# Kernel optimization log

Hardware: AMD Instinct MI355X
Metric: run time of the kernel (lower is better)

Reference implementation:

```python
import jax, jax.numpy as jnp
import numpy as np

N_NODES = 50000
N_EDGES = 800000
N_GRAPHS = 500
DIM = 64
RBF_DIM = 5      # ceil(cutoff/width) = ceil(5.0/1)
N_CONV = 3
N_TYPES = 100
CLS_DIM = 2000
CUTOFF = 5.0

def _w(key, shape, fan_in):
    return jax.random.normal(key, shape, dtype=jnp.float32) / np.sqrt(fan_in)

def setup_inputs() -> dict:
    key = jax.random.key(0)
    ks = jax.random.split(key, 16)
    return {
        "node_types": jax.random.randint(ks[0], (N_NODES,), 0, N_TYPES, dtype=jnp.int32),
        "edge_src": jax.random.randint(ks[1], (N_EDGES,), 0, N_NODES, dtype=jnp.int32),
        "edge_dst": jax.random.randint(ks[2], (N_EDGES,), 0, N_NODES, dtype=jnp.int32),
        "graph_ids": jnp.sort(jax.random.randint(ks[3], (N_NODES,), 0, N_GRAPHS, dtype=jnp.int32)),
        "distance": jax.random.uniform(ks[4], (N_EDGES,), dtype=jnp.float32) * CUTOFF,
        "emb": jax.random.normal(ks[5], (N_TYPES, DIM), dtype=jnp.float32),
        "conv_w1": _w(ks[6], (N_CONV, DIM, DIM), DIM),
        "cf1_w": _w(ks[7], (N_CONV, RBF_DIM, DIM), RBF_DIM),
        "cf1_b": jnp.zeros((N_CONV, DIM), jnp.float32),
        "cf2_w": _w(ks[8], (N_CONV, DIM, DIM), DIM),
        "cf2_b": jnp.zeros((N_CONV, DIM), jnp.float32),
        "nl2_w": _w(ks[9], (N_CONV, DIM, DIM), DIM),
        "nl2_b": jnp.zeros((N_CONV, DIM), jnp.float32),
        "nl3_w": _w(ks[10], (N_CONV, DIM, DIM), DIM),
        "nl3_b": jnp.zeros((N_CONV, DIM), jnp.float32),
        "d1_w": _w(ks[11], (DIM, 256), DIM),
        "d1_b": jnp.zeros((256,), jnp.float32),
        "d2_w": _w(ks[12], (256, 256), 256),
        "d2_b": jnp.zeros((256,), jnp.float32),
        "cls_w": _w(ks[13], (256, CLS_DIM), 256),
        "cls_b": jnp.zeros((CLS_DIM,), jnp.float32),
        "ac_w": _w(ks[14], (256, N_TYPES), 256),
        "ac_b": jnp.zeros((N_TYPES,), jnp.float32),
    }

def _sp2(x):
    # torch nn.Softplus(beta=0.5): (1/0.5) * log(1 + exp(0.5 * x))
    return 2.0 * jax.nn.softplus(0.5 * x)

def reference(node_types, edge_src, edge_dst, graph_ids, distance, emb,
              conv_w1, cf1_w, cf1_b, cf2_w, cf2_b, nl2_w, nl2_b, nl3_w, nl3_b,
              d1_w, d1_b, d2_w, d2_b, cls_w, cls_b, ac_w, ac_b):
    # RBF expansion of edge distances: centers = linspace(low, high, n_centers)
    centers = jnp.linspace(0.0, CUTOFF, RBF_DIM)
    gap = centers[1] - centers[0]
    rbf = jnp.exp(-(1.0 / gap) * (distance[:, None] - centers) ** 2)  # [E, RBF_DIM]

    node = emb[node_types]                                            # AtomEmbedding -> [N, D]
    for i in range(N_CONV):                                           # Interaction layers
        new_node = node @ conv_w1[i]                                  # Linear(dim, dim, bias=False)
        eh = _sp2(rbf @ cf1_w[i] + cf1_b[i])                          # CFConv filter network
        eh = _sp2(eh @ cf2_w[i] + cf2_b[i])                           # [E, D]
        msg = new_node[edge_src] * eh                                 # fn.u_mul_e gather
        agg = jax.ops.segment_sum(msg, edge_dst, num_segments=N_NODES)  # fn.sum scatter
        t = _sp2(agg @ nl2_w[i] + nl2_b[i])
        node = node + t @ nl3_w[i] + nl3_b[i]                         # residual update

    atom = node @ d1_w + d1_b
    atom = jax.nn.softplus(atom) - jnp.log(2.0)                       # ShiftSoftplus
    res = atom @ d2_w + d2_b                                          # [N, 256]
    atoms_preds = jax.nn.relu(res) @ ac_w + ac_b                      # [N, 100]

    ones = jnp.ones((N_NODES,), jnp.float32)
    counts = jax.ops.segment_sum(ones, graph_ids, num_segments=N_GRAPHS)
    emb_g = jax.ops.segment_sum(res, graph_ids, num_segments=N_GRAPHS) / jnp.maximum(counts, 1.0)[:, None]
    cls_preds = emb_g @ cls_w + cls_b                                 # [B, cls_dim]
    return atoms_preds, cls_preds
```

## Files before the change

kernel.cpp:

```cpp
#include <hip/hip_runtime.h>
#include <math.h>

#define N_NODES 50000
#define N_EDGES 800000
#define N_GRAPHS 500
#define DIM 64
#define RBF_DIM 5
#define N_CONV 3
#define CLS_DIM 2000
#define ACT_DIM 100
#define HID 256
#define TAB 2048
#define CAP 64

typedef __attribute__((ext_vector_type(8))) short bf16x8;
typedef __attribute__((ext_vector_type(4))) float f32x4;
#define MFMA16(a,b,c) __builtin_amdgcn_mfma_f32_16x16x32_bf16(a,b,c,0,0,0)

__device__ __forceinline__ float sp2f(float x){
    float y = 0.5f * x;
    return 2.0f * (fmaxf(y, 0.0f) + log1pf(__expf(-fabsf(y))));
}
__device__ __forceinline__ float sspf(float x){
    return fmaxf(x, 0.0f) + log1pf(__expf(-fabsf(x))) - 0.69314718055994531f;
}
__device__ __forceinline__ short f2b(float x){
    union { float f; unsigned u; } v; v.f = x;
    unsigned r = v.u + 0x7FFFu + ((v.u >> 16) & 1u);
    return (short)(r >> 16);
}
__device__ __forceinline__ float b2f(short x){
    union { unsigned u; float f; } v; v.u = ((unsigned)(unsigned short)x) << 16;
    return v.f;
}

__global__ void k_tw(const float* __restrict__ cw, const float* __restrict__ n2,
                     const float* __restrict__ n3, const float* __restrict__ d1w,
                     const float* __restrict__ d2w, const float* __restrict__ acw,
                     const float* __restrict__ clsw, const float* __restrict__ emb,
                     short* __restrict__ cwt, short* __restrict__ n2t, short* __restrict__ n3t,
                     short* __restrict__ d1t, short* __restrict__ d2t, short* __restrict__ act,
                     short* __restrict__ clswt, short* __restrict__ embw0b){
    int b = blockIdx.x, tid = threadIdx.x;
    if (b < 144){
        int i = b * 256 + tid;
        int y = i >> 12, j = i & 4095;
        int which = y / 3, layer = y % 3;
        const float* src = (which == 0 ? cw : which == 1 ? n2 : n3) + layer * 4096;
        short* dst = (which == 0 ? cwt : which == 1 ? n2t : n3t) + layer * 4096;
        int k = j >> 6, n = j & 63;
        dst[n * 64 + k] = f2b(src[k * 64 + n]);
    } else if (b < 208){
        int i = (b - 144) * 256 + tid;
        int k = i >> 8, n = i & 255;
        d1t[n * 64 + k] = f2b(d1w[k * 256 + n]);
    } else if (b < 464){
        int i = (b - 208) * 256 + tid;
        int k = i >> 8, n = i & 255;
        d2t[n * 256 + k] = f2b(d2w[k * 256 + n]);
    } else if (b < 576){
        int i = (b - 464) * 256 + tid;
        int n = i >> 8, k = i & 255;
        act[n * 256 + k] = f2b(n < ACT_DIM ? acw[k * ACT_DIM + n] : 0.f);
    } else if (b < 2624){
        int i = (b - 576) * 256 + tid;
        int k = i >> 11, n = i & 2047;
        clswt[n * 256 + k] = f2b(n < CLS_DIM ? clsw[k * CLS_DIM + n] : 0.f);
    } else {
        int i = (b - 2624) * 256 + tid;
        if (i < 100 * 64){
            int t = i >> 6, c = i & 63;
            float a = 0.f;
            #pragma unroll 8
            for (int k = 0; k < 64; ++k) a += emb[t * 64 + k] * cw[k * 64 + c];
            embw0b[i] = f2b(a);
        }
    }
}

__global__ void k_embed(const int* __restrict__ types, const float* __restrict__ emb,
                        const short* __restrict__ embw0b,
                        float* __restrict__ node, short* __restrict__ nodeb,
                        short* __restrict__ nnb,
                        const int* __restrict__ gid, float* __restrict__ counts){
    int i = blockIdx.x * 256 + threadIdx.x;
    if (i < N_NODES * DIM){
        int t = types[i >> 6], c = i & 63;
        float v = emb[t * 64 + c];
        node[i] = v; nodeb[i] = f2b(v);
        nnb[i] = embw0b[t * 64 + c];
    }
    if (i < N_NODES) atomicAdd(&counts[gid[i]], 1.0f);
}

__global__ void k_scatter2(const int* __restrict__ esrc, const int* __restrict__ edst,
                           const float* __restrict__ dist, int* __restrict__ cnt,
                           float2* __restrict__ edata2){
    int e = blockIdx.x * 256 + threadIdx.x;
    if (e >= N_EDGES) return;
    int d = edst[e];
    int pos = atomicAdd(&cnt[d], 1);
    if (pos < CAP) edata2[d * CAP + pos] = make_float2(dist[e], __int_as_float(esrc[e]));
}

__global__ __launch_bounds__(256) void k_table3(const float* __restrict__ cf1w_all,
    const float* __restrict__ cf1b_all, const float* __restrict__ cf2w_all,
    const float* __restrict__ cf2b_all, short* __restrict__ tabb_all)
{
    int L = blockIdx.y;
    const float* cf1w = cf1w_all + L * RBF_DIM * DIM;
    const float* cf1b = cf1b_all + L * DIM;
    const float* cf2w = cf2w_all + L * DIM * DIM;
    const float* cf2b = cf2b_all + L * DIM;
    short* tabb = tabb_all + L * TAB * 64;
    __shared__ float s_cf1[RBF_DIM * 64];
    __shared__ float s_cf1b[64], s_cf2b[64];
    __shared__ float s_cf2[64 * 64];
    __shared__ float s_h1[4 * 64];
    int tid = threadIdx.x;
    int c = tid & 63, g = tid >> 6;
    for (int i = tid; i < 64 * 64; i += 256) s_cf2[i] = cf2w[i];
    for (int i = tid; i < RBF_DIM * 64; i += 256) s_cf1[i] = cf1w[i];
    if (tid < 64){ s_cf1b[tid] = cf1b[tid]; s_cf2b[tid] = cf2b[tid]; }
    __syncthreads();
    int entry = blockIdx.x * 4 + g;
    float d = (float)entry * (5.0f / (float)(TAB - 1));
    {
        float acc = s_cf1b[c];
        #pragma unroll
        for (int j = 0; j < RBF_DIM; ++j){
            float t = d - 1.25f * (float)j;
            acc += __expf(-0.8f * t * t) * s_cf1[j * 64 + c];
        }
        s_h1[g * 64 + c] = sp2f(acc);
    }
    __syncthreads();
    {
        float acc = s_cf2b[c];
        #pragma unroll 8
        for (int k = 0; k < 64; ++k) acc += s_h1[g * 64 + k] * s_cf2[k * 64 + c];
        tabb[entry * 64 + c] = f2b(sp2f(acc));
    }
}

__global__ void k_pack(const short* __restrict__ tabb_all, unsigned* __restrict__ tabp_all){
    int L = blockIdx.y;
    int i = blockIdx.x * 256 + threadIdx.x;
    if (i < (TAB - 1) * 64){
        int t = i >> 6, c = i & 63;
        unsigned lo = (unsigned short)tabb_all[L * TAB * 64 + t * 64 + c];
        unsigned hi = (unsigned short)tabb_all[L * TAB * 64 + (t + 1) * 64 + c];
        tabp_all[L * TAB * 64 + t * 64 + c] = lo | (hi << 16);
    }
}

__global__ __launch_bounds__(256) void k_agg(const float2* __restrict__ edata2,
    const int* __restrict__ cnt, const unsigned* __restrict__ tabp,
    const short* __restrict__ nnb, short* __restrict__ aggb)
{
    const float SC = (float)(TAB - 1) / 5.0f;
    int tid = threadIdx.x;
    int c = tid & 63, r = tid >> 6;
    int n = blockIdx.x * 4 + r;
    if (n >= N_NODES) return;
    int m = min(cnt[n], CAP);
    const float2* ed = edata2 + (long)n * CAP;
    float acc = 0.f;
    int e = 0;
    for (; e + 4 <= m; e += 4){
        float2 ev0 = ed[e], ev1 = ed[e+1], ev2 = ed[e+2], ev3 = ed[e+3];
        int s0 = __float_as_int(ev0.y), s1 = __float_as_int(ev1.y);
        int s2 = __float_as_int(ev2.y), s3 = __float_as_int(ev3.y);
        float x0 = ev0.x * SC; int i0 = min((int)x0, TAB - 2); float f0 = x0 - (float)i0;
        float x1 = ev1.x * SC; int i1 = min((int)x1, TAB - 2); float f1 = x1 - (float)i1;
        float x2 = ev2.x * SC; int i2 = min((int)x2, TAB - 2); float f2 = x2 - (float)i2;
        float x3 = ev3.x * SC; int i3 = min((int)x3, TAB - 2); float f3 = x3 - (float)i3;
        unsigned u0 = tabp[i0 * 64 + c], u1 = tabp[i1 * 64 + c];
        unsigned u2 = tabp[i2 * 64 + c], u3 = tabp[i3 * 64 + c];
        float n0 = b2f(nnb[s0 * 64 + c]), n1 = b2f(nnb[s1 * 64 + c]);
        float n2 = b2f(nnb[s2 * 64 + c]), n3 = b2f(nnb[s3 * 64 + c]);
        float w00 = __uint_as_float(u0 << 16), w01 = __uint_as_float(u0 & 0xffff0000u);
        float w10 = __uint_as_float(u1 << 16), w11 = __uint_as_float(u1 & 0xffff0000u);
        float w20 = __uint_as_float(u2 << 16), w21 = __uint_as_float(u2 & 0xffff0000u);
        float w30 = __uint_as_float(u3 << 16), w31 = __uint_as_float(u3 & 0xffff0000u);
        acc += n0 * (w00 + (w01 - w00) * f0);
        acc += n1 * (w10 + (w11 - w10) * f1);
        acc += n2 * (w20 + (w21 - w20) * f2);
        acc += n3 * (w30 + (w31 - w30) * f3);
    }
    for (; e < m; ++e){
        float2 ev = ed[e];
        int s = __float_as_int(ev.y);
        float x = ev.x * SC; int i0 = min((int)x, TAB - 2); float f = x - (float)i0;
        unsigned u = tabp[i0 * 64 + c];
        float w0 = __uint_as_float(u << 16), w1 = __uint_as_float(u & 0xffff0000u);
        acc += b2f(nnb[s * 64 + c]) * (w0 + (w1 - w0) * f);
    }
    aggb[n * 64 + c] = f2b(acc);
}

__global__ __launch_bounds__(256) void k_update(const short* __restrict__ aggb,
    const short* __restrict__ nl2t, const float* __restrict__ nl2b,
    const short* __restrict__ nl3t, const float* __restrict__ nl3b,
    float* __restrict__ node, short* __restrict__ nodeb,
    const short* __restrict__ wnext, short* __restrict__ nnb)
{
    __shared__ short sT[32 * 80];
    int tid = threadIdx.x, wave = tid >> 6, lane = tid & 63;
    int quad = lane >> 4, l16 = lane & 15;
    int row0 = blockIdx.x * 32;
    int rt = wave >> 1;
    int ctb = (wave & 1) * 2;
    f32x4 acc[2] = {{0,0,0,0},{0,0,0,0}};
    #pragma unroll
    for (int kt = 0; kt < 2; ++kt){
        int k0 = kt * 32 + quad * 8;
        int rw = row0 + rt * 16 + l16;
        bf16x8 a = (rw < N_NODES) ? *(const bf16x8*)&aggb[rw * 64 + k0] : (bf16x8){0,0,0,0,0,0,0,0};
        #pragma unroll
        for (int i = 0; i < 2; ++i){
            bf16x8 b = *(const bf16x8*)&nl2t[((ctb + i) * 16 + l16) * 64 + k0];
            acc[i] = MFMA16(a, b, acc[i]);
        }
    }
    #pragma unroll
    for (int i = 0; i < 2; ++i)
        #pragma unroll
        for (int reg = 0; reg < 4; ++reg){
            int rl = rt * 16 + quad * 4 + reg;
            int col = (ctb + i) * 16 + l16;
            sT[rl * 80 + col] = f2b(sp2f(acc[i][reg] + nl2b[col]));
        }
    __syncthreads();
    f32x4 acc2[2] = {{0,0,0,0},{0,0,0,0}};
    #pragma unroll
    for (int kt = 0; kt < 2; ++kt){
        int k0 = kt * 32 + quad * 8;
        bf16x8 a = *(const bf16x8*)&sT[(rt * 16 + l16) * 80 + k0];
        #pragma unroll
        for (int i = 0; i < 2; ++i){
            bf16x8 b = *(const bf16x8*)&nl3t[((ctb + i) * 16 + l16) * 64 + k0];
            acc2[i] = MFMA16(a, b, acc2[i]);
        }
    }
    short vb[2][4];
    #pragma unroll
    for (int i = 0; i < 2; ++i)
        #pragma unroll
        for (int reg = 0; reg < 4; ++reg){
            int row = row0 + rt * 16 + quad * 4 + reg;
            int col = (ctb + i) * 16 + l16;
            float v = 0.f;
            if (row < N_NODES){
                v = node[row * 64 + col] + acc2[i][reg] + nl3b[col];
                node[row * 64 + col] = v;
            }
            short vbs = f2b(v);
            vb[i][reg] = vbs;
            if (row < N_NODES) nodeb[row * 64 + col] = vbs;
        }
    if (wnext){
        __syncthreads();
        #pragma unroll
        for (int i = 0; i < 2; ++i)
            #pragma unroll
            for (int reg = 0; reg < 4; ++reg)
                sT[(rt * 16 + quad * 4 + reg) * 80 + (ctb + i) * 16 + l16] = vb[i][reg];
        __syncthreads();
        f32x4 acc3[2] = {{0,0,0,0},{0,0,0,0}};
        #pragma unroll
        for (int kt = 0; kt < 2; ++kt){
            int k0 = kt * 32 + quad * 8;
            bf16x8 a = *(const bf16x8*)&sT[(rt * 16 + l16) * 80 + k0];
            #pragma unroll
            for (int i = 0; i < 2; ++i){
                bf16x8 b = *(const bf16x8*)&wnext[((ctb + i) * 16 + l16) * 64 + k0];
                acc3[i] = MFMA16(a, b, acc3[i]);
            }
        }
        #pragma unroll
        for (int i = 0; i < 2; ++i)
            #pragma unroll
            for (int reg = 0; reg < 4; ++reg){
                int row = row0 + rt * 16 + quad * 4 + reg;
                int col = (ctb + i) * 16 + l16;
                if (row < N_NODES) nnb[row * 64 + col] = f2b(acc3[i][reg]);
            }
    }
}

__global__ __launch_bounds__(256) void k_r1(const short* __restrict__ nodeb,
    const short* __restrict__ d1t, const float* __restrict__ d1b,
    short* __restrict__ atomb)
{
    int tid = threadIdx.x, wave = tid >> 6, lane = tid & 63;
    int quad = lane >> 4, l16 = lane & 15;
    int row0 = blockIdx.x * 32;
    f32x4 acc[2][4] = {{{0,0,0,0},{0,0,0,0},{0,0,0,0},{0,0,0,0}},
                       {{0,0,0,0},{0,0,0,0},{0,0,0,0},{0,0,0,0}}};
    #pragma unroll
    for (int kt = 0; kt < 2; ++kt){
        int k0 = kt * 32 + quad * 8;
        bf16x8 a[2];
        #pragma unroll
        for (int rt = 0; rt < 2; ++rt){
            int rw = row0 + rt * 16 + l16;
            a[rt] = (rw < N_NODES) ? *(const bf16x8*)&nodeb[rw * 64 + k0] : (bf16x8){0,0,0,0,0,0,0,0};
        }
        #pragma unroll
        for (int ct = 0; ct < 4; ++ct){
            int n = wave * 64 + ct * 16 + l16;
            bf16x8 b = *(const bf16x8*)&d1t[n * 64 + k0];
            #pragma unroll
            for (int rt = 0; rt < 2; ++rt) acc[rt][ct] = MFMA16(a[rt], b, acc[rt][ct]);
        }
    }
    #pragma unroll
    for (int rt = 0; rt < 2; ++rt)
        #pragma unroll
        for (int ct = 0; ct < 4; ++ct){
            int col = wave * 64 + ct * 16 + l16;
            float bb = d1b[col];
            #pragma unroll
            for (int reg = 0; reg < 4; ++reg){
                int row = row0 + rt * 16 + quad * 4 + reg;
                if (row < N_NODES) atomb[row * HID + col] = f2b(sspf(acc[rt][ct][reg] + bb));
            }
        }
}

__global__ __launch_bounds__(256) void k_r2(const short* __restrict__ atomb,
    const short* __restrict__ d2t, const float* __restrict__ d2b_,
    const int* __restrict__ gid, float* __restrict__ gacc, short* __restrict__ resb)
{
    __shared__ float sres[32 * 260];
    int tid = threadIdx.x, wave = tid >> 6, lane = tid & 63;
    int quad = lane >> 4, l16 = lane & 15;
    int row0 = blockIdx.x * 32;
    f32x4 acc[2][4] = {{{0,0,0,0},{0,0,0,0},{0,0,0,0},{0,0,0,0}},
                       {{0,0,0,0},{0,0,0,0},{0,0,0,0},{0,0,0,0}}};
    for (int kt = 0; kt < 8; ++kt){
        int k0 = kt * 32 + quad * 8;
        bf16x8 a[2];
        #pragma unroll
        for (int rt = 0; rt < 2; ++rt){
            int rw = row0 + rt * 16 + l16;
            a[rt] = (rw < N_NODES) ? *(const bf16x8*)&atomb[rw * HID + k0] : (bf16x8){0,0,0,0,0,0,0,0};
        }
        #pragma unroll
        for (int ct = 0; ct < 4; ++ct){
            int n = wave * 64 + ct * 16 + l16;
            bf16x8 b = *(const bf16x8*)&d2t[n * HID + k0];
            #pragma unroll
            for (int rt = 0; rt < 2; ++rt) acc[rt][ct] = MFMA16(a[rt], b, acc[rt][ct]);
        }
    }
    #pragma unroll
    for (int rt = 0; rt < 2; ++rt)
        #pragma unroll
        for (int ct = 0; ct < 4; ++ct){
            int col = wave * 64 + ct * 16 + l16;
            float bb = d2b_[col];
            #pragma unroll
            for (int reg = 0; reg < 4; ++reg){
                int rl = rt * 16 + quad * 4 + reg;
                sres[rl * 260 + col] = acc[rt][ct][reg] + bb;
            }
        }
    __syncthreads();
    float run = 0.f; int cur = -1;
    for (int r = 0; r < 32; ++r){
        int n = row0 + r;
        if (n >= N_NODES) break;
        float v = sres[r * 260 + tid];
        int g = gid[n];
        if (g != cur){
            if (cur >= 0) atomicAdd(&gacc[cur * HID + tid], run);
            run = 0.f; cur = g;
        }
        run += v;
        resb[n * HID + tid] = f2b(fmaxf(v, 0.f));
    }
    if (cur >= 0) atomicAdd(&gacc[cur * HID + tid], run);
}

__global__ __launch_bounds__(256) void k_r3(const short* __restrict__ resb,
    const short* __restrict__ act, const float* __restrict__ acb,
    float* __restrict__ out_atoms)
{
    int tid = threadIdx.x, wave = tid >> 6, lane = tid & 63;
    int quad = lane >> 4, l16 = lane & 15;
    int row0 = blockIdx.x * 64;
    f32x4 acc[7] = {{0,0,0,0},{0,0,0,0},{0,0,0,0},{0,0,0,0},{0,0,0,0},{0,0,0,0},{0,0,0,0}};
    for (int kt = 0; kt < 8; ++kt){
        int k0 = kt * 32 + quad * 8;
        int rw = row0 + wave * 16 + l16;
        bf16x8 a = (rw < N_NODES) ? *(const bf16x8*)&resb[rw * HID + k0] : (bf16x8){0,0,0,0,0,0,0,0};
        #pragma unroll
        for (int ct = 0; ct < 7; ++ct){
            bf16x8 b = *(const bf16x8*)&act[(ct * 16 + l16) * HID + k0];
            acc[ct] = MFMA16(a, b, acc[ct]);
        }
    }
    #pragma unroll
    for (int ct = 0; ct < 7; ++ct){
        int col = ct * 16 + l16;
        if (col >= ACT_DIM) continue;
        float bb = acb[col];
        #pragma unroll
        for (int reg = 0; reg < 4; ++reg){
            int row = row0 + wave * 16 + quad * 4 + reg;
            if (row < N_NODES) out_atoms[row * ACT_DIM + col] = acc[ct][reg] + bb;
        }
    }
}

__global__ void k_embg(const float* __restrict__ gacc, const float* __restrict__ counts,
                       short* __restrict__ gclsb){
    int i = blockIdx.x * 256 + threadIdx.x;
    if (i < N_GRAPHS * HID){
        int g = i >> 8;
        gclsb[i] = f2b(gacc[i] / fmaxf(counts[g], 1.0f));
    }
}

__global__ __launch_bounds__(256) void k_cls2(const short* __restrict__ gclsb,
    const short* __restrict__ clswt, const float* __restrict__ clsb,
    float* __restrict__ out_cls)
{
    int tid = threadIdx.x, wave = tid >> 6, lane = tid & 63;
    int quad = lane >> 4, l16 = lane & 15;
    int row0 = blockIdx.x * 32;
    int colbase = blockIdx.y * 256 + wave * 64;
    f32x4 acc[2][4] = {{{0,0,0,0},{0,0,0,0},{0,0,0,0},{0,0,0,0}},
                       {{0,0,0,0},{0,0,0,0},{0,0,0,0},{0,0,0,0}}};
    for (int kt = 0; kt < 8; ++kt){
        int k0 = kt * 32 + quad * 8;
        bf16x8 a[2];
        #pragma unroll
        for (int rt = 0; rt < 2; ++rt){
            int rw = row0 + rt * 16 + l16;
            a[rt] = (rw < N_GRAPHS) ? *(const bf16x8*)&gclsb[rw * HID + k0] : (bf16x8){0,0,0,0,0,0,0,0};
        }
        #pragma unroll
        for (int ct = 0; ct < 4; ++ct){
            bf16x8 b = *(const bf16x8*)&clswt[(colbase + ct * 16 + l16) * HID + k0];
            #pragma unroll
            for (int rt = 0; rt < 2; ++rt) acc[rt][ct] = MFMA16(a[rt], b, acc[rt][ct]);
        }
    }
    #pragma unroll
    for (int rt = 0; rt < 2; ++rt)
        #pragma unroll
        for (int ct = 0; ct < 4; ++ct){
            int col = colbase + ct * 16 + l16;
            if (col >= CLS_DIM) continue;
            float bb = clsb[col];
            #pragma unroll
            for (int reg = 0; reg < 4; ++reg){
                int row = row0 + rt * 16 + quad * 4 + reg;
                if (row < N_GRAPHS) out_cls[row * CLS_DIM + col] = acc[rt][ct][reg] + bb;
            }
        }
}

extern "C" void kernel_launch(void* const* d_in, const int* in_sizes, int n_in,
                              void* d_out, int out_size, void* d_ws, size_t ws_size,
                              hipStream_t stream)
{
    const int*   node_types = (const int*)d_in[0];
    const int*   edge_src   = (const int*)d_in[1];
    const int*   edge_dst   = (const int*)d_in[2];
    const int*   graph_ids  = (const int*)d_in[3];
    const float* distance   = (const float*)d_in[4];
    const float* emb        = (const float*)d_in[5];
    const float* conv_w1    = (const float*)d_in[6];
    const float* cf1_w      = (const float*)d_in[7];
    const float* cf1_b      = (const float*)d_in[8];
    const float* cf2_w      = (const float*)d_in[9];
    const float* cf2_b      = (const float*)d_in[10];
    const float* nl2_w      = (const float*)d_in[11];
    const float* nl2_b      = (const float*)d_in[12];
    const float* nl3_w      = (const float*)d_in[13];
    const float* nl3_b      = (const float*)d_in[14];
    const float* d1_w       = (const float*)d_in[15];
    const float* d1_b       = (const float*)d_in[16];
    const float* d2_w       = (const float*)d_in[17];
    const float* d2_b       = (const float*)d_in[18];
    const float* cls_w      = (const float*)d_in[19];
    const float* cls_b      = (const float*)d_in[20];
    const float* ac_w       = (const float*)d_in[21];
    const float* ac_b       = (const float*)d_in[22];

    float*    node   = (float*)d_ws;
    float*    gacc   = node + 3200000;
    float*    counts = gacc + 128000;
    float2*   edata2 = (float2*)(counts + 512);
    int*      cnt    = (int*)(edata2 + 3200000);
    short*    nodeb  = (short*)(cnt + 50048);
    short*    nnb    = nodeb + 3200000;
    short*    aggb   = nnb + 3200000;
    short*    tabb   = aggb + 3200000;
    unsigned* tabp   = (unsigned*)(tabb + 3 * 131072);
    short*    cw1t   = (short*)(tabp + 3 * 131072);
    short*    n2t    = cw1t + 12288;
    short*    n3t    = n2t + 12288;
    short*    d1t    = n3t + 12288;
    short*    d2t    = d1t + 16384;
    short*    act    = d2t + 65536;
    short*    clswt  = act + 28672;
    short*    gclsb  = clswt + 524288;
    short*    embw0b = gclsb + 128000;
    short*    atomb  = (short*)edata2;
    short*    resb   = atomb;
    float*    out    = (float*)d_out;

    (void)hipMemsetAsync(gacc, 0, (128000 + 512) * sizeof(float), stream);
    (void)hipMemsetAsync(cnt, 0, 50048 * sizeof(int), stream);

    k_tw<<<2649, 256, 0, stream>>>(conv_w1, nl2_w, nl3_w, d1_w, d2_w, ac_w, cls_w, emb,
                                   cw1t, n2t, n3t, d1t, d2t, act, clswt, embw0b);
    k_table3<<<dim3(TAB / 4, 3), 256, 0, stream>>>(cf1_w, cf1_b, cf2_w, cf2_b, tabb);
    k_pack<<<dim3(512, 3), 256, 0, stream>>>(tabb, tabp);

    k_embed<<<(N_NODES * DIM + 255) / 256, 256, 0, stream>>>(node_types, emb, embw0b,
        node, nodeb, nnb, graph_ids, counts);
    k_scatter2<<<(N_EDGES + 255) / 256, 256, 0, stream>>>(edge_src, edge_dst, distance,
                                                          cnt, edata2);

    for (int i = 0; i < N_CONV; ++i){
        k_agg<<<(N_NODES + 3) / 4, 256, 0, stream>>>(edata2, cnt, tabp + i * TAB * 64,
                                                     nnb, aggb);
        k_update<<<(N_NODES + 31) / 32, 256, 0, stream>>>(aggb,
            n2t + i * 4096, nl2_b + i * DIM, n3t + i * 4096, nl3_b + i * DIM,
            node, nodeb, (i < N_CONV - 1) ? (cw1t + (i + 1) * 4096) : (const short*)nullptr, nnb);
    }

    k_r1<<<(N_NODES + 31) / 32, 256, 0, stream>>>(nodeb, d1t, d1_b, atomb);
    k_r2<<<(N_NODES + 31) / 32, 256, 0, stream>>>(atomb, d2t, d2_b, graph_ids, gacc, resb);
    k_r3<<<(N_NODES + 63) / 64, 256, 0, stream>>>(resb, act, ac_b, out);
    k_embg<<<(N_GRAPHS * HID + 255) / 256, 256, 0, stream>>>(gacc, counts, gclsb);
    k_cls2<<<dim3((N_GRAPHS + 31) / 32, (CLS_DIM + 255) / 256), 256, 0, stream>>>(
        gclsb, clswt, cls_b, out + N_NODES * ACT_DIM);
}
```

Measured before the change: 532.1 us.

## Pack edge data into 32-bit words and broadcast via wave shuffles

Edge records are compressed from a float2 (distance, src) into one 32-bit word holding a 15-bit fixed-point table coordinate and a 17-bit source index. In the aggregation kernel each lane loads one record and the wave shares them with shuffles, instead of every lane reading every record. The edge scatter is also fused into the embedding kernel, the two memsets are merged, and the workspace is re-laid out. This cuts edge-list bandwidth and per-lane redundant loads and removes one launch, at the cost of quantizing distance to 1/16 of a table step.

```diff
diff --git a/kernel.cpp b/kernel.cpp
--- a/kernel.cpp
+++ b/kernel.cpp
@@ -82,7 +82,10 @@
                         const short* __restrict__ embw0b,
                         float* __restrict__ node, short* __restrict__ nodeb,
                         short* __restrict__ nnb,
-                        const int* __restrict__ gid, float* __restrict__ counts){
+                        const int* __restrict__ gid, float* __restrict__ counts,
+                        const int* __restrict__ esrc, const int* __restrict__ edst,
+                        const float* __restrict__ dist,
+                        int* __restrict__ cnt, unsigned* __restrict__ edata){
     int i = blockIdx.x * 256 + threadIdx.x;
     if (i < N_NODES * DIM){
         int t = types[i >> 6], c = i & 63;
@@ -90,17 +93,17 @@
         node[i] = v; nodeb[i] = f2b(v);
         nnb[i] = embw0b[t * 64 + c];
     }
+    if (i < N_EDGES){
+        int d = edst[i];
+        int pos = atomicAdd(&cnt[d], 1);
+        if (pos < CAP){
+            const float SC16 = (float)(TAB - 1) * 16.0f / 5.0f;
+            int v = (int)(dist[i] * SC16 + 0.5f);
+            v = min(v, 32767);
+            edata[d * CAP + pos] = ((unsigned)v << 17) | (unsigned)esrc[i];
+        }
+    }
     if (i < N_NODES) atomicAdd(&counts[gid[i]], 1.0f);
-}
-
-__global__ void k_scatter2(const int* __restrict__ esrc, const int* __restrict__ edst,
-                           const float* __restrict__ dist, int* __restrict__ cnt,
-                           float2* __restrict__ edata2){
-    int e = blockIdx.x * 256 + threadIdx.x;
-    if (e >= N_EDGES) return;
-    int d = edst[e];
-    int pos = atomicAdd(&cnt[d], 1);
-    if (pos < CAP) edata2[d * CAP + pos] = make_float2(dist[e], __int_as_float(esrc[e]));
 }
 
 __global__ __launch_bounds__(256) void k_table3(const float* __restrict__ cf1w_all,
@@ -154,44 +157,49 @@
     }
 }
 
-__global__ __launch_bounds__(256) void k_agg(const float2* __restrict__ edata2,
+__global__ __launch_bounds__(256) void k_agg(const unsigned* __restrict__ edata,
     const int* __restrict__ cnt, const unsigned* __restrict__ tabp,
     const short* __restrict__ nnb, short* __restrict__ aggb)
 {
-    const float SC = (float)(TAB - 1) / 5.0f;
     int tid = threadIdx.x;
     int c = tid & 63, r = tid >> 6;
     int n = blockIdx.x * 4 + r;
     if (n >= N_NODES) return;
     int m = min(cnt[n], CAP);
-    const float2* ed = edata2 + (long)n * CAP;
+    const unsigned* ed = edata + (long)n * CAP;
+    unsigned ev = (c < m) ? ed[c] : 0u;
+    int s_l = (int)(ev & 0x1FFFFu);
+    int v_l = (int)(ev >> 17);
+    int i0_l = min(v_l >> 4, TAB - 2);
+    float f_l = (float)(v_l - (i0_l << 4)) * 0.0625f;
+    int pk_l = (i0_l << 17) | s_l;
     float acc = 0.f;
     int e = 0;
     for (; e + 4 <= m; e += 4){
-        float2 ev0 = ed[e], ev1 = ed[e+1], ev2 = ed[e+2], ev3 = ed[e+3];
-        int s0 = __float_as_int(ev0.y), s1 = __float_as_int(ev1.y);
-        int s2 = __float_as_int(ev2.y), s3 = __float_as_int(ev3.y);
-        float x0 = ev0.x * SC; int i0 = min((int)x0, TAB - 2); float f0 = x0 - (float)i0;
-        float x1 = ev1.x * SC; int i1 = min((int)x1, TAB - 2); float f1 = x1 - (float)i1;
-        float x2 = ev2.x * SC; int i2 = min((int)x2, TAB - 2); float f2 = x2 - (float)i2;
-        float x3 = ev3.x * SC; int i3 = min((int)x3, TAB - 2); float f3 = x3 - (float)i3;
-        unsigned u0 = tabp[i0 * 64 + c], u1 = tabp[i1 * 64 + c];
-        unsigned u2 = tabp[i2 * 64 + c], u3 = tabp[i3 * 64 + c];
-        float n0 = b2f(nnb[s0 * 64 + c]), n1 = b2f(nnb[s1 * 64 + c]);
-        float n2 = b2f(nnb[s2 * 64 + c]), n3 = b2f(nnb[s3 * 64 + c]);
-        float w00 = __uint_as_float(u0 << 16), w01 = __uint_as_float(u0 & 0xffff0000u);
-        float w10 = __uint_as_float(u1 << 16), w11 = __uint_as_float(u1 & 0xffff0000u);
-        float w20 = __uint_as_float(u2 << 16), w21 = __uint_as_float(u2 & 0xffff0000u);
-        float w30 = __uint_as_float(u3 << 16), w31 = __uint_as_float(u3 & 0xffff0000u);
-        acc += n0 * (w00 + (w01 - w00) * f0);
-        acc += n1 * (w10 + (w11 - w10) * f1);
-        acc += n2 * (w20 + (w21 - w20) * f2);
-        acc += n3 * (w30 + (w31 - w30) * f3);
+        int   pa = __shfl(pk_l, e);     float fa = __shfl(f_l, e);
+        int   pb = __shfl(pk_l, e + 1); float fb = __shfl(f_l, e + 1);
+        int   pc = __shfl(pk_l, e + 2); float fc = __shfl(f_l, e + 2);
+        int   pd = __shfl(pk_l, e + 3); float fd = __shfl(f_l, e + 3);
+        int ia = pa >> 17, sa = pa & 0x1FFFF;
+        int ib = pb >> 17, sb = pb & 0x1FFFF;
+        int ic = pc >> 17, sc = pc & 0x1FFFF;
+        int id = pd >> 17, sd = pd & 0x1FFFF;
+        unsigned ua = tabp[ia * 64 + c], ub = tabp[ib * 64 + c];
+        unsigned uc = tabp[ic * 64 + c], ud = tabp[id * 64 + c];
+        float na = b2f(nnb[sa * 64 + c]), nb = b2f(nnb[sb * 64 + c]);
+        float nc = b2f(nnb[sc * 64 + c]), nd = b2f(nnb[sd * 64 + c]);
+        float wa0 = __uint_as_float(ua << 16), wa1 = __uint_as_float(ua & 0xffff0000u);
+        float wb0 = __uint_as_float(ub << 16), wb1 = __uint_as_float(ub & 0xffff0000u);
+        float wc0 = __uint_as_float(uc << 16), wc1 = __uint_as_float(uc & 0xffff0000u);
+        float wd0 = __uint_as_float(ud << 16), wd1 = __uint_as_float(ud & 0xffff0000u);
+        acc += na * (wa0 + (wa1 - wa0) * fa);
+        acc += nb * (wb0 + (wb1 - wb0) * fb);
+        acc += nc * (wc0 + (wc1 - wc0) * fc);
+        acc += nd * (wd0 + (wd1 - wd0) * fd);
     }
     for (; e < m; ++e){
-        float2 ev = ed[e];
-        int s = __float_as_int(ev.y);
-        float x = ev.x * SC; int i0 = min((int)x, TAB - 2); float f = x - (float)i0;
+        int   p = __shfl(pk_l, e); float f = __shfl(f_l, e);
+        int i0 = p >> 17, s = p & 0x1FFFF;
         unsigned u = tabp[i0 * 64 + c];
         float w0 = __uint_as_float(u << 16), w1 = __uint_as_float(u & 0xffff0000u);
         acc += b2f(nnb[s * 64 + c]) * (w0 + (w1 - w0) * f);
@@ -492,11 +500,9 @@
     const float* ac_w       = (const float*)d_in[21];
     const float* ac_b       = (const float*)d_in[22];
 
-    float*    node   = (float*)d_ws;
-    float*    gacc   = node + 3200000;
+    float*    gacc   = (float*)d_ws;
     float*    counts = gacc + 128000;
-    float2*   edata2 = (float2*)(counts + 512);
-    int*      cnt    = (int*)(edata2 + 3200000);
+    int*      cnt    = (int*)(counts + 512);
     short*    nodeb  = (short*)(cnt + 50048);
     short*    nnb    = nodeb + 3200000;
     short*    aggb   = nnb + 3200000;
@@ -511,12 +517,13 @@
     short*    clswt  = act + 28672;
     short*    gclsb  = clswt + 524288;
     short*    embw0b = gclsb + 128000;
-    short*    atomb  = (short*)edata2;
+    float*    node   = (float*)(embw0b + 6400);
+    unsigned* edata  = (unsigned*)(node + 3200000);
+    short*    atomb  = (short*)node;
     short*    resb   = atomb;
     float*    out    = (float*)d_out;
 
-    (void)hipMemsetAsync(gacc, 0, (128000 + 512) * sizeof(float), stream);
-    (void)hipMemsetAsync(cnt, 0, 50048 * sizeof(int), stream);
+    (void)hipMemsetAsync(gacc, 0, (128000 + 512) * sizeof(float) + 50048 * sizeof(int), stream);
 
     k_tw<<<2649, 256, 0, stream>>>(conv_w1, nl2_w, nl3_w, d1_w, d2_w, ac_w, cls_w, emb,
                                    cw1t, n2t, n3t, d1t, d2t, act, clswt, embw0b);
@@ -524,12 +531,10 @@
     k_pack<<<dim3(512, 3), 256, 0, stream>>>(tabb, tabp);
 
     k_embed<<<(N_NODES * DIM + 255) / 256, 256, 0, stream>>>(node_types, emb, embw0b,
-        node, nodeb, nnb, graph_ids, counts);
-    k_scatter2<<<(N_EDGES + 255) / 256, 256, 0, stream>>>(edge_src, edge_dst, distance,
-                                                          cnt, edata2);
+        node, nodeb, nnb, graph_ids, counts, edge_src, edge_dst, distance, cnt, edata);
 
     for (int i = 0; i < N_CONV; ++i){
-        k_agg<<<(N_NODES + 3) / 4, 256, 0, stream>>>(edata2, cnt, tabp + i * TAB * 64,
+        k_agg<<<(N_NODES + 3) / 4, 256, 0, stream>>>(edata, cnt, tabp + i * TAB * 64,
                                                      nnb, aggb);
         k_update<<<(N_NODES + 31) / 32, 256, 0, stream>>>(aggb,
             n2t + i * 4096, nl2_b + i * DIM, n3t + i * 4096, nl3_b + i * DIM,
```

Result: faster. 492.8 us (-7.4%).
